# Performance work log

Measured on AMD Instinct MI355X. Metric: run time of the kernel, lower is better.

The kernel has to match this reference:

```python
import jax, jax.numpy as jnp
import numpy as np

N = 50000          # nodes
E = 800000         # edges (avg in-degree 16)
F = 128            # hidden_dim
AVG_LOG = float(np.log(17.0))  # PyG avg_deg['log'] from deg histogram concentrated at degree 16
BN_EPS = 1e-5
STD_EPS = 1e-5


def setup_inputs() -> dict:
    key = jax.random.key(0)
    ks = jax.random.split(key, 10)
    h = jax.random.normal(ks[0], (N, F), dtype=jnp.float32)
    edge_index = jax.random.randint(ks[1], (2, E), 0, N, dtype=jnp.int64)

    def lin_w(k, fan_in, fan_out):
        return jax.random.normal(k, (fan_in, fan_out), dtype=jnp.float32) / np.sqrt(fan_in)

    return {
        "h": h,
        "edge_index": edge_index,
        "W_pre": lin_w(ks[2], 2 * F, F),   # pre_nn: Linear(2F -> F) on [x_i, x_j]
        "b_pre": jnp.zeros((F,), jnp.float32),
        "W_post": lin_w(ks[3], 13 * F, F),  # post_nn: Linear((1 + 4*3)F -> F)
        "b_post": jnp.zeros((F,), jnp.float32),
        "W_lin": lin_w(ks[4], F, F),       # final Linear(F -> F)
        "b_lin": jnp.zeros((F,), jnp.float32),
        "gamma": jnp.ones((F,), jnp.float32),   # BatchNorm1d weight
        "beta": jnp.zeros((F,), jnp.float32),   # BatchNorm1d bias
    }


def reference(h, edge_index, W_pre, b_pre, W_post, b_post, W_lin, b_lin, gamma, beta):
    src = edge_index[0]  # x_j (message source)
    dst = edge_index[1]  # x_i (aggregation target)
    n = h.shape[0]

    # pre_nn on concat([x_i, x_j])  -> per-edge message [E, F]
    m = jnp.concatenate([h[dst], h[src]], axis=-1) @ W_pre + b_pre

    # multi-aggregator scatter: mean, min, max, std (PyG order)
    cnt = jax.ops.segment_sum(jnp.ones((m.shape[0],), m.dtype), dst, num_segments=n)  # [N]
    deg = jnp.maximum(cnt, 1.0)[:, None]                                              # clamp(1)
    mean = jax.ops.segment_sum(m, dst, num_segments=n) / deg
    mean_sq = jax.ops.segment_sum(m * m, dst, num_segments=n) / deg
    std = jnp.sqrt(jax.nn.relu(mean_sq - mean * mean) + STD_EPS)
    has = (cnt > 0)[:, None]
    mn = jnp.where(has, jax.ops.segment_min(m, dst, num_segments=n), 0.0)
    mx = jnp.where(has, jax.ops.segment_max(m, dst, num_segments=n), 0.0)
    aggr = jnp.concatenate([mean, mn, mx, std], axis=-1)  # [N, 4F]

    # degree scalers: identity, amplification, attenuation
    logd = jnp.log(deg + 1.0)
    out = jnp.concatenate(
        [aggr, aggr * (logd / AVG_LOG), aggr * (AVG_LOG / logd)], axis=-1
    )  # [N, 12F]

    # update: concat self features, post_nn, final lin
    out = jnp.concatenate([h, out], axis=-1) @ W_post + b_post  # [N, F]
    out = out @ W_lin + b_lin

    # BatchNorm1d (training-mode batch statistics, biased variance) + ReLU
    mu = out.mean(axis=0)
    var = out.var(axis=0)
    out = (out - mu) / jnp.sqrt(var + BN_EPS) * gamma + beta
    out = jax.nn.relu(out)
    # dropout p=0.0 is identity; residual add
    return out + h
```

## Files before the change

### kernel.cpp

```cpp
#include <hip/hip_runtime.h>
#include <hip/hip_bf16.h>
#include <cstdint>
#include <cstddef>

typedef short s16x8 __attribute__((ext_vector_type(8)));
typedef float f32x4 __attribute__((ext_vector_type(4)));

#define AVG_LOG_F 2.8332133f

static __device__ __forceinline__ float b2f(unsigned short u) {
  union { unsigned int i; float f; } x; x.i = ((unsigned int)u) << 16; return x.f;
}
static __device__ __forceinline__ unsigned short f2b(float f) {
  __hip_bfloat16 h = __float2bfloat16(f);
  union { __hip_bfloat16 hh; unsigned short u; } c; c.hh = h; return c.u;
}
static __device__ __forceinline__ unsigned int pack2(float lo, float hi) {
  return (unsigned int)f2b(lo) | ((unsigned int)f2b(hi) << 16);
}
static __device__ __forceinline__ uint4 cvt8(const float* p) {
  const float4 lo = *(const float4*)p;
  const float4 hi = *(const float4*)(p + 4);
  uint4 r;
  r.x = pack2(lo.x, lo.y); r.y = pack2(lo.z, lo.w);
  r.z = pack2(hi.x, hi.y); r.w = pack2(hi.z, hi.w);
  return r;
}
static __device__ __forceinline__ int swz(int row, int slot) {
  return row * 32 + ((slot ^ ((row >> 1) & 3)) << 3);
}

__global__ void fold_wcat_kernel(const float* __restrict__ W_pre, unsigned short* __restrict__ WcatT) {
  int idx = blockIdx.x * blockDim.x + threadIdx.x;
  int c = idx >> 7, k = idx & 127;
  float v = (c < 128) ? W_pre[k * 128 + c] : W_pre[(128 + k) * 128 + (c - 128)];
  WcatT[c * 128 + k] = f2b(v);
}

__global__ __launch_bounds__(128) void fold_wpost_kernel(
    const float* __restrict__ W_post, const float* __restrict__ b_post,
    const float* __restrict__ W_lin, const float* __restrict__ b_lin,
    unsigned short* __restrict__ WfoldT, float* __restrict__ bfold) {
  __shared__ float wl[128 * 128];
  const int j = threadIdx.x;
  for (int r = 0; r < 128; ++r) wl[r * 128 + j] = W_lin[r * 128 + j];
  __syncthreads();
  if (blockIdx.x == 208) {
    float acc = b_lin[j];
    for (int k = 0; k < 128; ++k) acc += b_post[k] * wl[k * 128 + j];
    bfold[j] = acc;
  } else {
#pragma unroll 2
    for (int ii = 0; ii < 8; ++ii) {
      const int i = blockIdx.x * 8 + ii;
      float acc = 0.f;
      for (int k = 0; k < 128; ++k) acc += W_post[i * 128 + k] * wl[k * 128 + j];
      WfoldT[(size_t)j * 1664 + i] = f2b(acc);
    }
  }
}

__global__ void bucket_hist_kernel(const int* __restrict__ dst, int* __restrict__ bucketCnt, int E) {
  __shared__ int lcnt[256];
  const int tid = threadIdx.x;
  lcnt[tid] = 0;
  __syncthreads();
  for (int e = blockIdx.x * 256 + tid; e < E; e += gridDim.x * 256)
    atomicAdd(&lcnt[dst[e] >> 8], 1);
  __syncthreads();
  if (lcnt[tid] > 0) atomicAdd(&bucketCnt[tid], lcnt[tid]);
}

__global__ void bucket_scan_kernel(const int* __restrict__ bucketCnt, int* __restrict__ bucketBase,
                                   int* __restrict__ bucketCursor, int* __restrict__ rowptr,
                                   int n, int nb, int E) {
  __shared__ int sh[256];
  const int tid = threadIdx.x;
  const int v = (tid < nb) ? bucketCnt[tid] : 0;
  sh[tid] = v;
  __syncthreads();
  for (int o = 1; o < 256; o <<= 1) {
    int t = (tid >= o) ? sh[tid - o] : 0;
    __syncthreads();
    sh[tid] += t;
    __syncthreads();
  }
  const int base = sh[tid] - v;
  if (tid < nb) { bucketBase[tid] = base; bucketCursor[tid] = base; }
  if (tid == nb - 1) bucketBase[nb] = base + v;
  if (tid == 0) rowptr[n] = E;
}

__global__ __launch_bounds__(256) void s1_scatter_kernel(
    const int* __restrict__ src, const int* __restrict__ dst,
    int* __restrict__ bucketCursor, unsigned int* __restrict__ bucketed, int E, int CH) {
  __shared__ int lcnt[256], loff[256], lcur[256], gbase[256];
  __shared__ unsigned int stage[5000];
  __shared__ unsigned char sbid[5000];
  const int tid = threadIdx.x;
  const int c0 = blockIdx.x * CH;
  const int c1 = min(c0 + CH, E);
  const int cnt = c1 - c0;
  if (cnt <= 0) return;
  lcnt[tid] = 0;
  __syncthreads();
  for (int e = c0 + tid; e < c1; e += 256) atomicAdd(&lcnt[dst[e] >> 8], 1);
  __syncthreads();
  const int v = lcnt[tid];
  loff[tid] = 0;
  __syncthreads();
  {
    __shared__ int tmp[256];
    tmp[tid] = v;
    __syncthreads();
    for (int o = 1; o < 256; o <<= 1) {
      int t = (tid >= o) ? tmp[tid - o] : 0;
      __syncthreads();
      tmp[tid] += t;
      __syncthreads();
    }
    loff[tid] = tmp[tid] - v;
  }
  lcur[tid] = loff[tid];
  gbase[tid] = (v > 0) ? atomicAdd(&bucketCursor[tid], v) : 0;
  __syncthreads();
  for (int e = c0 + tid; e < c1; e += 256) {
    const int d = dst[e];
    const int b = d >> 8;
    const int slot = atomicAdd(&lcur[b], 1);
    stage[slot] = ((unsigned int)(d & 255) << 16) | (unsigned int)src[e];
    sbid[slot] = (unsigned char)b;
  }
  __syncthreads();
  for (int i = tid; i < cnt; i += 256) {
    const int b = sbid[i];
    bucketed[gbase[b] + (i - loff[b])] = stage[i];
  }
}

__global__ __launch_bounds__(256) void s2_build_kernel(
    const unsigned int* __restrict__ bucketed, const int* __restrict__ bucketBase,
    int* __restrict__ rowptr, unsigned short* __restrict__ ssrc, int n) {
  __shared__ int ncnt[256], noff[256], ncur[256];
  __shared__ unsigned short csr16[8192];
  const int tid = threadIdx.x;
  const int b = blockIdx.x;
  const int seg0 = bucketBase[b], seg1 = bucketBase[b + 1];
  const int cnt = seg1 - seg0;
  ncnt[tid] = 0;
  __syncthreads();
  for (int i = tid; i < cnt; i += 256) atomicAdd(&ncnt[bucketed[seg0 + i] >> 16], 1);
  __syncthreads();
  const int v = ncnt[tid];
  {
    __shared__ int tmp[256];
    tmp[tid] = v;
    __syncthreads();
    for (int o = 1; o < 256; o <<= 1) {
      int t = (tid >= o) ? tmp[tid - o] : 0;
      __syncthreads();
      tmp[tid] += t;
      __syncthreads();
    }
    noff[tid] = tmp[tid] - v;
  }
  ncur[tid] = noff[tid];
  const int node = (b << 8) + tid;
  if (node < n) rowptr[node] = seg0 + noff[tid];
  __syncthreads();
  for (int i = tid; i < cnt; i += 256) {
    const unsigned int rec = bucketed[seg0 + i];
    const int d = rec >> 16;
    const int slot = atomicAdd(&ncur[d], 1);
    if (slot < 8192) csr16[slot] = (unsigned short)(rec & 0xffffu);
  }
  __syncthreads();
  for (int i = tid; i < cnt; i += 256) ssrc[seg0 + i] = csr16[i];
}

__global__ __launch_bounds__(256) void gemm256_kernel(
    const float* __restrict__ A, const unsigned short* __restrict__ BT,
    unsigned short* __restrict__ outb, int M)
{
  constexpr int LDT = 40;
  constexpr int K = 128, NK = K / 32;
  __shared__ alignas(16) unsigned short Asm[2][128 * LDT];
  __shared__ alignas(16) unsigned short Bsm[2][128 * LDT];
  const int tid = threadIdx.x, lane = tid & 63;
  const int w = tid >> 6, wr = w >> 1, wc = w & 1;
  const int row0 = blockIdx.x * 128;
  const int col0 = blockIdx.y * 128;
  const int srow = tid >> 2, slot = tid & 3;
  const int ar0 = min(row0 + srow, M - 1);
  const int ar1 = min(row0 + srow + 64, M - 1);
  const float* ap0 = A + (size_t)ar0 * K + slot * 8;
  const float* ap1 = A + (size_t)ar1 * K + slot * 8;
  const unsigned short* bp0 = BT + (size_t)(col0 + srow) * K + slot * 8;
  const unsigned short* bp1 = BT + (size_t)(col0 + srow + 64) * K + slot * 8;
  const int wa0 = srow * LDT + slot * 8, wa1 = wa0 + 64 * LDT;

  int offA[4], offB[4];
#pragma unroll
  for (int i = 0; i < 4; ++i) {
    offA[i] = (wr * 64 + i * 16 + (lane & 15)) * LDT + (lane >> 4) * 8;
    offB[i] = (wc * 64 + i * 16 + (lane & 15)) * LDT + (lane >> 4) * 8;
  }

  f32x4 acc[4][4] = {};
  uint4 a0 = cvt8(ap0);
  uint4 a1 = cvt8(ap1);
  uint4 b0 = *(const uint4*)bp0;
  uint4 b1 = *(const uint4*)bp1;
  *(uint4*)&Asm[0][wa0] = a0; *(uint4*)&Asm[0][wa1] = a1;
  *(uint4*)&Bsm[0][wa0] = b0; *(uint4*)&Bsm[0][wa1] = b1;
  __syncthreads();

  for (int kt = 0; kt < NK; ++kt) {
    const int cur = kt & 1;
    if (kt + 1 < NK) {
      const int k0 = (kt + 1) * 32;
      a0 = cvt8(ap0 + k0); a1 = cvt8(ap1 + k0);
      b0 = *(const uint4*)(bp0 + k0); b1 = *(const uint4*)(bp1 + k0);
    }
    s16x8 af[4], bq[4];
#pragma unroll
    for (int i = 0; i < 4; ++i) af[i] = *(const s16x8*)&Asm[cur][offA[i]];
#pragma unroll
    for (int i = 0; i < 4; ++i) bq[i] = *(const s16x8*)&Bsm[cur][offB[i]];
#pragma unroll
    for (int mi = 0; mi < 4; ++mi)
#pragma unroll
      for (int ni = 0; ni < 4; ++ni)
        acc[mi][ni] = __builtin_amdgcn_mfma_f32_16x16x32_bf16(af[mi], bq[ni], acc[mi][ni], 0, 0, 0);
    if (kt + 1 < NK) {
      const int nxt = cur ^ 1;
      *(uint4*)&Asm[nxt][wa0] = a0; *(uint4*)&Asm[nxt][wa1] = a1;
      *(uint4*)&Bsm[nxt][wa0] = b0; *(uint4*)&Bsm[nxt][wa1] = b1;
      __syncthreads();
    }
  }

#pragma unroll
  for (int mi = 0; mi < 4; ++mi) {
#pragma unroll
    for (int ni = 0; ni < 4; ++ni) {
      const int rbase = row0 + wr * 64 + mi * 16 + (lane >> 4) * 4;
      const int c = col0 + wc * 64 + ni * 16 + (lane & 15);
#pragma unroll
      for (int r = 0; r < 4; ++r) {
        const int rr = rbase + r;
        if (rr < M) outb[(size_t)rr * 256 + c] = f2b(acc[mi][ni][r]);
      }
    }
  }
}

#define AGG_EDGE(IDX)                                                                  \
  {                                                                                    \
    const unsigned int v = *(const unsigned int*)(AB + (size_t)(IDX) * 256 + 128 + 2 * lane); \
    const float v0 = b2f((unsigned short)(v & 0xffffu));                               \
    const float v1 = b2f((unsigned short)(v >> 16));                                   \
    s0 += v0; q0 += v0 * v0; mn0 = fminf(mn0, v0); mx0 = fmaxf(mx0, v0);               \
    s1v += v1; q1 += v1 * v1; mn1 = fminf(mn1, v1); mx1 = fmaxf(mx1, v1);              \
  }

__global__ void aggregate_kernel(const unsigned short* __restrict__ AB,
                                 const float* __restrict__ h,
                                 const float* __restrict__ b_pre,
                                 const int* __restrict__ rowptr, const unsigned short* __restrict__ ssrc,
                                 unsigned short* __restrict__ Xagg,
                                 float* __restrict__ sc1, float* __restrict__ sc2, int n) {
  const int node = blockIdx.x * 4 + (threadIdx.x >> 6);
  if (node >= n) return;
  const int lane = threadIdx.x & 63;
  const int beg = rowptr[node], end = rowptr[node + 1];
  const int cnt = end - beg;
  float s0 = 0.f, s1v = 0.f, q0 = 0.f, q1 = 0.f;
  float mn0 = 3.4e38f, mn1 = 3.4e38f, mx0 = -3.4e38f, mx1 = -3.4e38f;
  for (int base = beg; base < end; base += 64) {
    const int m = min(64, end - base);
    const int myidx = (base + lane < end) ? (int)ssrc[base + lane] : 0;
    int t = 0;
    for (; t + 8 <= m; t += 8) {
      const int i0 = __builtin_amdgcn_readlane(myidx, t + 0);
      const int i1 = __builtin_amdgcn_readlane(myidx, t + 1);
      const int i2 = __builtin_amdgcn_readlane(myidx, t + 2);
      const int i3 = __builtin_amdgcn_readlane(myidx, t + 3);
      const int i4 = __builtin_amdgcn_readlane(myidx, t + 4);
      const int i5 = __builtin_amdgcn_readlane(myidx, t + 5);
      const int i6 = __builtin_amdgcn_readlane(myidx, t + 6);
      const int i7 = __builtin_amdgcn_readlane(myidx, t + 7);
      AGG_EDGE(i0) AGG_EDGE(i1) AGG_EDGE(i2) AGG_EDGE(i3)
      AGG_EDGE(i4) AGG_EDGE(i5) AGG_EDGE(i6) AGG_EDGE(i7)
    }
    for (; t < m; ++t) {
      const int i0 = __builtin_amdgcn_readlane(myidx, t);
      AGG_EDGE(i0)
    }
  }
  const float degf = (float)(cnt > 0 ? cnt : 1);
  const float2 bp = ((const float2*)b_pre)[lane];
  const unsigned int cpair = *(const unsigned int*)(AB + (size_t)node * 256 + 2 * lane);
  const float c0 = b2f((unsigned short)(cpair & 0xffffu)) + bp.x;
  const float c1 = b2f((unsigned short)(cpair >> 16)) + bp.y;
  float mean0, mean1, std0, std1, lo0, lo1, hi0, hi1;
  if (cnt > 0) {
    const float inv = 1.f / degf;
    const float mu0 = s0 * inv, mu1 = s1v * inv;
    mean0 = c0 + mu0; mean1 = c1 + mu1;
    std0 = sqrtf(fmaxf(q0 * inv - mu0 * mu0, 0.f) + 1e-5f);
    std1 = sqrtf(fmaxf(q1 * inv - mu1 * mu1, 0.f) + 1e-5f);
    lo0 = c0 + mn0; lo1 = c1 + mn1; hi0 = c0 + mx0; hi1 = c1 + mx1;
  } else {
    mean0 = mean1 = lo0 = lo1 = hi0 = hi1 = 0.f;
    std0 = std1 = sqrtf(1e-5f);
  }
  const float logd = logf(degf + 1.f);
  const float2 hv = ((const float2*)(h + (size_t)node * 128))[lane];
  unsigned int* row = (unsigned int*)(Xagg + (size_t)node * 640);
  row[lane]       = pack2(hv.x, hv.y);
  row[64 + lane]  = pack2(mean0, mean1);
  row[128 + lane] = pack2(lo0, lo1);
  row[192 + lane] = pack2(hi0, hi1);
  row[256 + lane] = pack2(std0, std1);
  if (lane == 0) { sc1[node] = logd / AVG_LOG_F; sc2[node] = AVG_LOG_F / logd; }
}

static __device__ __forceinline__ uint4 scale8(uint4 r, float s) {
  union { uint4 v; unsigned short h[8]; } in, out;
  in.v = r;
#pragma unroll
  for (int i = 0; i < 8; ++i) out.h[i] = f2b(b2f(in.h[i]) * s);
  return out.v;
}
static __device__ __forceinline__ uint4 loadA_fold(const unsigned short* base, int kc,
                                                   float s1v, float s2v) {
  const bool m1 = kc >= 640;
  const bool m2 = kc >= 1152;
  const int off = kc - (m1 ? 512 : 0) - (m2 ? 512 : 0);
  uint4 r = *(const uint4*)(base + off);
  if (m1) r = scale8(r, m2 ? s2v : s1v);
  return r;
}

#define FOLD_MFMA(CUR)                                                              \
  {                                                                                 \
    s16x8 af[4], bq[2];                                                             \
    _Pragma("unroll") for (int i = 0; i < 4; ++i)                                   \
        af[i] = *(const s16x8*)&Asm[CUR][offA[i]];                                  \
    _Pragma("unroll") for (int i = 0; i < 2; ++i)                                   \
        bq[i] = *(const s16x8*)&Bsm[CUR][offB[i]];                                  \
    _Pragma("unroll") for (int mi = 0; mi < 4; ++mi)                                \
      _Pragma("unroll") for (int ni = 0; ni < 2; ++ni)                              \
        acc[mi][ni] = __builtin_amdgcn_mfma_f32_16x16x32_bf16(af[mi], bq[ni],       \
                                                              acc[mi][ni], 0, 0, 0);\
  }

__global__ __launch_bounds__(512) void gemm_fold2_kernel(
    const unsigned short* __restrict__ Xagg, const float* __restrict__ sc1,
    const float* __restrict__ sc2, const unsigned short* __restrict__ WT,
    const float* __restrict__ bias, float* __restrict__ out3,
    float* __restrict__ bnsum, int M)
{
  constexpr int NK = 52;
  __shared__ alignas(16) unsigned short Asm[2][128 * 32];
  __shared__ alignas(16) unsigned short Bsm[2][128 * 32];
  __shared__ float bnacc[256];
  const int tid = threadIdx.x, lane = tid & 63, w = tid >> 6;
  const int wr = w >> 2, wc = w & 3;
  const int row0 = blockIdx.x * 128;
  const int srow = tid >> 2, slot = tid & 3;
  const int arow = min(row0 + srow, M - 1);
  const unsigned short* abase = Xagg + (size_t)arow * 640;
  const unsigned short* bbase = WT + (size_t)srow * 1664 + slot * 8;
  const float s1v = sc1[arow], s2v = sc2[arow];
  const int wa = swz(srow, slot);
  if (tid < 256) bnacc[tid] = 0.f;

  int offA[4], offB[2];
#pragma unroll
  for (int i = 0; i < 4; ++i) offA[i] = swz(wr * 64 + i * 16 + (lane & 15), lane >> 4);
#pragma unroll
  for (int i = 0; i < 2; ++i) offB[i] = swz(wc * 32 + i * 16 + (lane & 15), lane >> 4);

  f32x4 acc[4][2] = {};
  {
    uint4 a = loadA_fold(abase, slot * 8, s1v, s2v);
    uint4 b = *(const uint4*)bbase;
    *(uint4*)&Asm[0][wa] = a;
    *(uint4*)&Bsm[0][wa] = b;
  }
  uint4 aS1 = loadA_fold(abase, 32 + slot * 8, s1v, s2v);
  uint4 bS1 = *(const uint4*)(bbase + 32);
  uint4 aS0, bS0;
  __syncthreads();

  for (int kt = 0; kt < NK; kt += 2) {
    {
      const int k2 = min(kt + 2, NK - 1) * 32;
      aS0 = loadA_fold(abase, k2 + slot * 8, s1v, s2v);
      bS0 = *(const uint4*)(bbase + k2);
      FOLD_MFMA(0)
      *(uint4*)&Asm[1][wa] = aS1;
      *(uint4*)&Bsm[1][wa] = bS1;
      __syncthreads();
    }
    {
      const int k3 = min(kt + 3, NK - 1) * 32;
      aS1 = loadA_fold(abase, k3 + slot * 8, s1v, s2v);
      bS1 = *(const uint4*)(bbase + k3);
      FOLD_MFMA(1)
      if (kt + 2 < NK) {
        *(uint4*)&Asm[0][wa] = aS0;
        *(uint4*)&Bsm[0][wa] = bS0;
        __syncthreads();
      }
    }
  }

  float cs[2] = {0.f, 0.f}, css[2] = {0.f, 0.f};
#pragma unroll
  for (int mi = 0; mi < 4; ++mi) {
#pragma unroll
    for (int ni = 0; ni < 2; ++ni) {
      const int rbase = row0 + wr * 64 + mi * 16 + (lane >> 4) * 4;
      const int c = wc * 32 + ni * 16 + (lane & 15);
      const float bb = bias[c];
#pragma unroll
      for (int r = 0; r < 4; ++r) {
        const int rr = rbase + r;
        if (rr < M) {
          const float v = acc[mi][ni][r] + bb;
          out3[(size_t)rr * 128 + c] = v;
          cs[ni] += v; css[ni] += v * v;
        }
      }
    }
  }
  __syncthreads();
#pragma unroll
  for (int ni = 0; ni < 2; ++ni) {
    const int c = wc * 32 + ni * 16 + (lane & 15);
    atomicAdd(&bnacc[c], cs[ni]);
    atomicAdd(&bnacc[128 + c], css[ni]);
  }
  __syncthreads();
  if (tid < 128) {
    atomicAdd(&bnsum[tid], bnacc[tid]);
    atomicAdd(&bnsum[128 + tid], bnacc[128 + tid]);
  }
}

__global__ void epilogue_kernel(const float* __restrict__ out3, const float* __restrict__ h,
                                const float* __restrict__ bnsum, const float* __restrict__ gamma,
                                const float* __restrict__ beta, float* __restrict__ out,
                                int n, int total4) {
  int i = blockIdx.x * blockDim.x + threadIdx.x;
  if (i >= total4) return;
  const int c = (i & 31) * 4;
  const float inv = 1.f / (float)n;
  const float4 x = ((const float4*)out3)[i];
  const float4 hh = ((const float4*)h)[i];
  float4 r;
  float* rp = (float*)&r;
  const float* xp = (const float*)&x;
  const float* hp = (const float*)&hh;
#pragma unroll
  for (int j = 0; j < 4; ++j) {
    const int cc = c + j;
    const float mu = bnsum[cc] * inv;
    const float var = bnsum[128 + cc] * inv - mu * mu;
    const float s = gamma[cc] * rsqrtf(var + 1e-5f);
    const float sh = beta[cc] - mu * s;
    rp[j] = fmaxf(xp[j] * s + sh, 0.f) + hp[j];
  }
  ((float4*)out)[i] = r;
}

extern "C" void kernel_launch(void* const* d_in, const int* in_sizes, int n_in,
                              void* d_out, int out_size, void* d_ws, size_t ws_size,
                              hipStream_t stream) {
  const float* h      = (const float*)d_in[0];
  const int*   ei     = (const int*)d_in[1];
  const float* W_pre  = (const float*)d_in[2];
  const float* b_pre  = (const float*)d_in[3];
  const float* W_post = (const float*)d_in[4];
  const float* b_post = (const float*)d_in[5];
  const float* W_lin  = (const float*)d_in[6];
  const float* b_lin  = (const float*)d_in[7];
  const float* gamma  = (const float*)d_in[8];
  const float* beta   = (const float*)d_in[9];

  const int n = in_sizes[0] / 128;
  const int E = in_sizes[1] / 2;
  const int* src = ei;
  const int* dst = ei + E;

  char* ws = (char*)d_ws;
  size_t off = 0;
  auto carve = [&](size_t bytes) {
    off = (off + 255) & ~(size_t)255;
    void* p = ws + off;
    off += bytes;
    return p;
  };
  void* ab_out3        = carve((size_t)n * 256 * 2);
  unsigned short* AB   = (unsigned short*)ab_out3;
  float* out3          = (float*)ab_out3;
  unsigned short* Xagg = (unsigned short*)carve((size_t)n * 640 * 2);
  float* sc1           = (float*)carve((size_t)n * 4);
  float* sc2           = (float*)carve((size_t)n * 4);
  unsigned short* WcatT  = (unsigned short*)carve(256 * 128 * 2);
  unsigned short* WfoldT = (unsigned short*)carve((size_t)128 * 1664 * 2);
  float* bfold         = (float*)carve(128 * 4);
  int*   bucketCnt     = (int*)carve(256 * 4);
  int*   bucketBase    = (int*)carve(257 * 4);
  int*   bucketCursor  = (int*)carve(256 * 4);
  unsigned int* bucketed = (unsigned int*)carve((size_t)E * 4);
  int*   rowptr        = (int*)carve((size_t)(n + 1) * 4);
  unsigned short* ssrc = (unsigned short*)carve((size_t)(E + 2) * 2);
  float* bnsum         = (float*)carve(256 * 4);

  const int total4 = n * 128 / 4;
  const int mt = (n + 127) / 128;
  const int nb = (n + 255) >> 8;
  const int nS1 = (E + 4999) / 5000;

  fold_wcat_kernel<<<128, 256, 0, stream>>>(W_pre, WcatT);
  fold_wpost_kernel<<<209, 128, 0, stream>>>(W_post, b_post, W_lin, b_lin, WfoldT, bfold);

  hipMemsetAsync(bucketCnt, 0, 256 * 4, stream);
  hipMemsetAsync(bnsum, 0, 256 * 4, stream);
  bucket_hist_kernel<<<256, 256, 0, stream>>>(dst, bucketCnt, E);
  bucket_scan_kernel<<<1, 256, 0, stream>>>(bucketCnt, bucketBase, bucketCursor, rowptr, n, nb, E);
  s1_scatter_kernel<<<nS1, 256, 0, stream>>>(src, dst, bucketCursor, bucketed, E, 5000);
  s2_build_kernel<<<nb, 256, 0, stream>>>(bucketed, bucketBase, rowptr, ssrc, n);

  gemm256_kernel<<<dim3(mt, 2), 256, 0, stream>>>(h, WcatT, AB, n);
  aggregate_kernel<<<(n + 3) / 4, 256, 0, stream>>>(AB, h, b_pre, rowptr, ssrc, Xagg, sc1, sc2, n);
  gemm_fold2_kernel<<<mt, 512, 0, stream>>>(Xagg, sc1, sc2, WfoldT, bfold, out3, bnsum, n);

  epilogue_kernel<<<(total4 + 255) / 256, 256, 0, stream>>>(out3, h, bnsum, gamma, beta,
                                                            (float*)d_out, n, total4);
}
```

Before: 287.0 us.

## Deepen fold-GEMM prefetch to two stages and defer scaling to LDS write

The fold GEMM loop now holds two K-tiles of global loads in flight as raw registers. The degree-scaler multiply is applied only when a tile is written to LDS, so the scaling no longer blocks right after the load. The LDS write for the next tile is issued before the MFMAs of the current tile. __syncthreads is replaced by an explicit lgkmcnt wait plus s_barrier, so outstanding global loads are not drained at each barrier. This adds register pressure and relies on hand-written wait semantics staying correct.

```diff
diff --git a/kernel.cpp b/kernel.cpp
--- a/kernel.cpp
+++ b/kernel.cpp
@@ -333,13 +333,12 @@
   for (int i = 0; i < 8; ++i) out.h[i] = f2b(b2f(in.h[i]) * s);
   return out.v;
 }
-static __device__ __forceinline__ uint4 loadA_fold(const unsigned short* base, int kc,
-                                                   float s1v, float s2v) {
-  const bool m1 = kc >= 640;
-  const bool m2 = kc >= 1152;
-  const int off = kc - (m1 ? 512 : 0) - (m2 ? 512 : 0);
-  uint4 r = *(const uint4*)(base + off);
-  if (m1) r = scale8(r, m2 ? s2v : s1v);
+static __device__ __forceinline__ const unsigned short* foldPtr(const unsigned short* base, int kc) {
+  return base + kc - (kc >= 640 ? 512 : 0) - (kc >= 1152 ? 512 : 0);
+}
+static __device__ __forceinline__ uint4 scaleA(uint4 r, int kc, float s1v, float s2v) {
+  if (kc >= 1152) return scale8(r, s2v);
+  if (kc >= 640)  return scale8(r, s1v);
   return r;
 }
 
@@ -385,35 +384,46 @@
 
   f32x4 acc[4][2] = {};
   {
-    uint4 a = loadA_fold(abase, slot * 8, s1v, s2v);
+    const int kc0 = slot * 8;
+    uint4 a = scaleA(*(const uint4*)foldPtr(abase, kc0), kc0, s1v, s2v);
     uint4 b = *(const uint4*)bbase;
     *(uint4*)&Asm[0][wa] = a;
     *(uint4*)&Bsm[0][wa] = b;
   }
-  uint4 aS1 = loadA_fold(abase, 32 + slot * 8, s1v, s2v);
-  uint4 bS1 = *(const uint4*)(bbase + 32);
-  uint4 aS0, bS0;
-  __syncthreads();
+  uint4 pa1 = *(const uint4*)foldPtr(abase, 32 + slot * 8);
+  uint4 pb1 = *(const uint4*)(bbase + 32);
+  uint4 pa0 = *(const uint4*)foldPtr(abase, 64 + slot * 8);
+  uint4 pb0 = *(const uint4*)(bbase + 64);
+  asm volatile("s_waitcnt lgkmcnt(0)" ::: "memory");
+  __builtin_amdgcn_s_barrier();
 
   for (int kt = 0; kt < NK; kt += 2) {
     {
-      const int k2 = min(kt + 2, NK - 1) * 32;
-      aS0 = loadA_fold(abase, k2 + slot * 8, s1v, s2v);
-      bS0 = *(const uint4*)(bbase + k2);
+      const int kcw = (kt + 1) * 32 + slot * 8;
+      uint4 aw = scaleA(pa1, kcw, s1v, s2v);
+      *(uint4*)&Asm[1][wa] = aw;
+      *(uint4*)&Bsm[1][wa] = pb1;
+      const int kt3 = min(kt + 3, NK - 1);
+      pa1 = *(const uint4*)foldPtr(abase, kt3 * 32 + slot * 8);
+      pb1 = *(const uint4*)(bbase + kt3 * 32);
       FOLD_MFMA(0)
-      *(uint4*)&Asm[1][wa] = aS1;
-      *(uint4*)&Bsm[1][wa] = bS1;
-      __syncthreads();
+      asm volatile("s_waitcnt lgkmcnt(0)" ::: "memory");
+      __builtin_amdgcn_s_barrier();
     }
     {
-      const int k3 = min(kt + 3, NK - 1) * 32;
-      aS1 = loadA_fold(abase, k3 + slot * 8, s1v, s2v);
-      bS1 = *(const uint4*)(bbase + k3);
-      FOLD_MFMA(1)
       if (kt + 2 < NK) {
-        *(uint4*)&Asm[0][wa] = aS0;
-        *(uint4*)&Bsm[0][wa] = bS0;
-        __syncthreads();
+        const int kcw = (kt + 2) * 32 + slot * 8;
+        uint4 aw = scaleA(pa0, kcw, s1v, s2v);
+        *(uint4*)&Asm[0][wa] = aw;
+        *(uint4*)&Bsm[0][wa] = pb0;
+        const int kt4 = min(kt + 4, NK - 1);
+        pa0 = *(const uint4*)foldPtr(abase, kt4 * 32 + slot * 8);
+        pb0 = *(const uint4*)(bbase + kt4 * 32);
+        FOLD_MFMA(1)
+        asm volatile("s_waitcnt lgkmcnt(0)" ::: "memory");
+        __builtin_amdgcn_s_barrier();
+      } else {
+        FOLD_MFMA(1)
       }
     }
   }
```

Measured after the change: 281.7 us. About the same (-1.8%).
